# Kernel optimization log

Measured on AMD Instinct MI355X. Metric: run time of the kernel, lower is better.

Reference implementation:

```python
import jax, jax.numpy as jnp
import numpy as np

D_MODEL = 1024
NUM_HEADS = 16
DEPTH = D_MODEL // NUM_HEADS
B, S = 2, 2048


def setup_inputs() -> dict:
    key = jax.random.key(0)
    ks = jax.random.split(key, 11)
    s = 1.0 / np.sqrt(D_MODEL)
    return {
        "v": jax.random.normal(ks[0], (B, S, D_MODEL), jnp.float32),
        "k": jax.random.normal(ks[1], (B, S, D_MODEL), jnp.float32),
        "q": jax.random.normal(ks[2], (B, S, D_MODEL), jnp.float32),
        "wq": jax.random.normal(ks[3], (D_MODEL, D_MODEL), jnp.float32) * s,
        "bq": jnp.zeros((D_MODEL,), jnp.float32),
        "wk": jax.random.normal(ks[4], (D_MODEL, D_MODEL), jnp.float32) * s,
        "bk": jnp.zeros((D_MODEL,), jnp.float32),
        "wv": jax.random.normal(ks[5], (D_MODEL, D_MODEL), jnp.float32) * s,
        "bv": jnp.zeros((D_MODEL,), jnp.float32),
        "wo": jax.random.normal(ks[6], (D_MODEL, D_MODEL), jnp.float32) * s,
        "bo": jnp.zeros((D_MODEL,), jnp.float32),
    }


def _split_heads(x):
    # [B, S, D] -> [B, H, S, depth]
    b, s, _ = x.shape
    return x.reshape(b, s, NUM_HEADS, DEPTH).transpose(0, 2, 1, 3)


def reference(v, k, q, wq, bq, wk, bk, wv, bv, wo, bo):
    qh = _split_heads(q @ wq + bq)
    kh = _split_heads(k @ wk + bk)
    vh = _split_heads(v @ wv + bv)
    scale = 1.0 / jnp.sqrt(jnp.asarray(DEPTH, jnp.float32))
    logits = jnp.einsum("bhqd,bhkd->bhqk", qh, kh) * scale
    attn = jax.nn.softmax(logits, axis=-1)
    out = jnp.einsum("bhqk,bhkd->bhqd", attn, vh)
    out = out.transpose(0, 2, 1, 3).reshape(q.shape[0], -1, D_MODEL)
    return out @ wo + bo
```

## Files before the change

kernel.cpp:

```cpp
#include <hip/hip_runtime.h>
#include <hip/hip_bf16.h>
#include <math.h>

#define DM   1024
#define SEQ  2048
#define NBAT 2
#define NH   16

typedef __attribute__((ext_vector_type(8)))  short short8;
typedef __attribute__((ext_vector_type(4)))  float f32x4;
typedef __attribute__((ext_vector_type(16))) float f32x16;
typedef unsigned short ushort_t;

#define QSCALE 0.1803368801111204f
#define DEFER_THR 11.541560327111708f

__device__ __forceinline__ unsigned short f2bf(float f) {
  unsigned int u = __float_as_uint(f);
  u += 0x7fff + ((u >> 16) & 1);
  return (unsigned short)(u >> 16);
}

__device__ __forceinline__ unsigned cvtpk(float lo, float hi) {
  unsigned r;
  asm("v_cvt_pk_bf16_f32 %0, %1, %2" : "=v"(r) : "v"(lo), "v"(hi));
  return r;
}

__device__ __forceinline__ short8 mk8(unsigned a, unsigned b, unsigned c, unsigned d) {
  union { unsigned u[4]; short8 s; } x;
  x.u[0] = a; x.u[1] = b; x.u[2] = c; x.u[3] = d;
  return x.s;
}

#define GLDS16(g, l)                                                            \
  __builtin_amdgcn_global_load_lds((const __attribute__((address_space(1))) void*)(g), \
                                   (__attribute__((address_space(3))) void*)(l), 16, 0, 0)

__global__ __launch_bounds__(256) void prep(
    const float* __restrict__ q, const float* __restrict__ k, const float* __restrict__ v,
    ushort_t* __restrict__ qb, ushort_t* __restrict__ kb, ushort_t* __restrict__ vb,
    const float* __restrict__ w0, const float* __restrict__ w1,
    const float* __restrict__ w2, const float* __restrict__ w3,
    ushort_t* __restrict__ o0, ushort_t* __restrict__ o1,
    ushort_t* __restrict__ o2, ushort_t* __restrict__ o3) {
  const int z = blockIdx.y;
  const int t = threadIdx.x;
  if (z < 3) {
    const float* s = z == 0 ? q : z == 1 ? k : v;
    ushort_t* d = z == 0 ? qb : z == 1 ? kb : vb;
    int i = (blockIdx.x * 256 + t) * 8;
    f32x4 a = *(const f32x4*)(s + i);
    f32x4 b = *(const f32x4*)(s + i + 4);
    short8 o;
    o[0] = (short)f2bf(a[0]); o[1] = (short)f2bf(a[1]);
    o[2] = (short)f2bf(a[2]); o[3] = (short)f2bf(a[3]);
    o[4] = (short)f2bf(b[0]); o[5] = (short)f2bf(b[1]);
    o[6] = (short)f2bf(b[2]); o[7] = (short)f2bf(b[3]);
    *(short8*)(d + i) = o;
  } else {
    if (blockIdx.x >= 1024) return;
    const float* W = z == 3 ? w0 : z == 4 ? w1 : z == 5 ? w2 : w3;
    ushort_t* Wt = z == 3 ? o0 : z == 4 ? o1 : z == 5 ? o2 : o3;
    __shared__ float tile[32][33];
    int bx = (blockIdx.x & 31) * 32;
    int by = (blockIdx.x >> 5) * 32;
    int tx = t & 31, ty = t >> 5;
#pragma unroll
    for (int i = 0; i < 4; ++i)
      tile[ty + i * 8][tx] = W[(size_t)(by + ty + i * 8) * DM + bx + tx];
    __syncthreads();
#pragma unroll
    for (int i = 0; i < 4; ++i)
      Wt[(size_t)(bx + ty + i * 8) * DM + by + tx] = f2bf(tile[tx][ty + i * 8]);
  }
}

__global__ __launch_bounds__(256) void gemm_qkv(
    const ushort_t* __restrict__ Xq, const ushort_t* __restrict__ Xk, const ushort_t* __restrict__ Xv,
    const ushort_t* __restrict__ Wq, const ushort_t* __restrict__ Wk, const ushort_t* __restrict__ Wv,
    const float* __restrict__ Bq, const float* __restrict__ Bk, const float* __restrict__ Bv,
    ushort_t* __restrict__ Oq, ushort_t* __restrict__ Ok, ushort_t* __restrict__ Ov) {
  const int z = blockIdx.z;
  const ushort_t* X  = z == 0 ? Xq : z == 1 ? Xk : Xv;
  const ushort_t* Wt = z == 0 ? Wq : z == 1 ? Wk : Wv;
  const float* bias  = z == 0 ? Bq : z == 1 ? Bk : Bv;

  __shared__ ushort_t As[128 * 64];
  __shared__ ushort_t Bs[128 * 64];
  const int t = threadIdx.x, l = t & 63, w = t >> 6;
  const int wr = w >> 1, wc = w & 1;
  const int fr = l & 15, fg = l >> 4;
  const int mb = blockIdx.x * 128, nb = blockIdx.y * 128;

  f32x4 acc[4][4] = {};
  const int srow = w * 8 + (l >> 3);
  const int gcol = (((l & 7) ^ ((l >> 3) & 7))) * 8;

  for (int kt = 0; kt < DM; kt += 64) {
#pragma unroll
    for (int i = 0; i < 4; ++i) {
      int row = i * 32 + srow;
      GLDS16(X  + (size_t)(mb + row) * DM + kt + gcol, &As[i * 2048 + w * 512]);
      GLDS16(Wt + (size_t)(nb + row) * DM + kt + gcol, &Bs[i * 2048 + w * 512]);
    }
    __syncthreads();
#pragma unroll
    for (int ks = 0; ks < 2; ++ks) {
      short8 af[4], bf[4];
#pragma unroll
      for (int mt = 0; mt < 4; ++mt) {
        int row = wr * 64 + mt * 16 + fr;
        af[mt] = *(const short8*)&As[row * 64 + (((ks << 2) | fg) ^ (fr & 7)) * 8];
      }
#pragma unroll
      for (int nt = 0; nt < 4; ++nt) {
        int row = wc * 64 + nt * 16 + fr;
        bf[nt] = *(const short8*)&Bs[row * 64 + (((ks << 2) | fg) ^ (fr & 7)) * 8];
      }
#pragma unroll
      for (int mt = 0; mt < 4; ++mt)
#pragma unroll
        for (int nt = 0; nt < 4; ++nt)
          acc[mt][nt] = __builtin_amdgcn_mfma_f32_16x16x32_bf16(af[mt], bf[nt], acc[mt][nt], 0, 0, 0);
    }
    __syncthreads();
  }

#pragma unroll
  for (int nt = 0; nt < 4; ++nt) {
    int n = nb + wc * 64 + nt * 16 + fr;
    float bn = bias[n];
#pragma unroll
    for (int mt = 0; mt < 4; ++mt) {
#pragma unroll
      for (int r = 0; r < 4; ++r) {
        int m = mb + wr * 64 + mt * 16 + fg * 4 + r;
        float v = acc[mt][nt][r] + bn;
        if (z == 0) {
          Oq[(size_t)m * DM + n] = f2bf(v * QSCALE);
        } else if (z == 1) {
          Ok[(size_t)m * DM + n] = f2bf(v);
        } else {
          int b = m >> 11, s = m & 2047;
          int h = n >> 6, d = n & 63;
          Ov[(((size_t)(b * NH + h) * 64 + d) * SEQ) + s] = f2bf(v);
        }
      }
    }
  }
}

__global__ __launch_bounds__(256) void gemm_o(const ushort_t* __restrict__ X,
                                              const ushort_t* __restrict__ Wt,
                                              const float* __restrict__ bias,
                                              float* __restrict__ out) {
  __shared__ ushort_t As[128 * 64];
  __shared__ ushort_t Bs[64 * 64];
  const int t = threadIdx.x, l = t & 63, w = t >> 6;
  const int fr = l & 15, fg = l >> 4;
  const int mb = blockIdx.x * 128, nb = blockIdx.y * 64;

  f32x4 acc[2][4] = {};
  const int srow = w * 8 + (l >> 3);
  const int gcol = (((l & 7) ^ ((l >> 3) & 7))) * 8;

  for (int kt = 0; kt < DM; kt += 64) {
#pragma unroll
    for (int i = 0; i < 4; ++i)
      GLDS16(X + (size_t)(mb + i * 32 + srow) * DM + kt + gcol, &As[i * 2048 + w * 512]);
#pragma unroll
    for (int i = 0; i < 2; ++i)
      GLDS16(Wt + (size_t)(nb + i * 32 + srow) * DM + kt + gcol, &Bs[i * 2048 + w * 512]);
    __syncthreads();
#pragma unroll
    for (int ks = 0; ks < 2; ++ks) {
      short8 af[2], bf[4];
#pragma unroll
      for (int mt = 0; mt < 2; ++mt) {
        int row = w * 32 + mt * 16 + fr;
        af[mt] = *(const short8*)&As[row * 64 + (((ks << 2) | fg) ^ (fr & 7)) * 8];
      }
#pragma unroll
      for (int nt = 0; nt < 4; ++nt) {
        int row = nt * 16 + fr;
        bf[nt] = *(const short8*)&Bs[row * 64 + (((ks << 2) | fg) ^ (fr & 7)) * 8];
      }
#pragma unroll
      for (int mt = 0; mt < 2; ++mt)
#pragma unroll
        for (int nt = 0; nt < 4; ++nt)
          acc[mt][nt] = __builtin_amdgcn_mfma_f32_16x16x32_bf16(af[mt], bf[nt], acc[mt][nt], 0, 0, 0);
    }
    __syncthreads();
  }

#pragma unroll
  for (int nt = 0; nt < 4; ++nt) {
    int n = nb + nt * 16 + fr;
    float bn = bias[n];
#pragma unroll
    for (int mt = 0; mt < 2; ++mt)
#pragma unroll
      for (int r = 0; r < 4; ++r) {
        int m = mb + w * 32 + mt * 16 + fg * 4 + r;
        out[(size_t)m * DM + n] = acc[mt][nt][r] + bn;
      }
  }
}

#define KPAD 72
#define KVELEM (64 * KPAD)
__global__ __launch_bounds__(256) void attn_fwd(const ushort_t* __restrict__ Qh,
                                                const ushort_t* __restrict__ Kh,
                                                const ushort_t* __restrict__ Vt,
                                                ushort_t* __restrict__ Oh) {
  __shared__ ushort_t Ks[2 * KVELEM];
  __shared__ ushort_t Vs[2 * KVELEM];

  const int t = threadIdx.x, l = t & 63, w = t >> 6;
  const int col = l & 31, hi = l >> 5;
  const int q0 = blockIdx.x * 128;
  const int bh = blockIdx.y;
  const int b = bh >> 4, h = bh & 15;

  const ushort_t* Qp = Qh + (size_t)b * SEQ * DM + h * 64;
  const ushort_t* Kp = Kh + (size_t)b * SEQ * DM + h * 64;
  const ushort_t* Vp = Vt + (size_t)bh * 64 * SEQ;

  const int qrow = q0 + w * 32 + col;
  short8 qf[4];
#pragma unroll
  for (int ds = 0; ds < 4; ++ds)
    qf[ds] = *(const short8*)(Qp + (size_t)qrow * DM + ds * 16 + hi * 8);

  float m_run = -INFINITY, l_run = 0.f;
  f32x16 oA = {}, oB = {};

  const int srow = t >> 3;
  const int scol = (t & 7) * 8;

  short8 k0r = *(const short8*)(Kp + (size_t)srow * DM + scol);
  short8 k1r = *(const short8*)(Kp + (size_t)(32 + srow) * DM + scol);
  short8 v0r = *(const short8*)(Vp + (size_t)srow * SEQ + scol);
  short8 v1r = *(const short8*)(Vp + (size_t)(32 + srow) * SEQ + scol);
  *(short8*)&Ks[srow * KPAD + scol] = k0r;
  *(short8*)&Ks[(32 + srow) * KPAD + scol] = k1r;
  *(short8*)&Vs[srow * KPAD + scol] = v0r;
  *(short8*)&Vs[(32 + srow) * KPAD + scol] = v1r;
  k0r = *(const short8*)(Kp + (size_t)(64 + srow) * DM + scol);
  k1r = *(const short8*)(Kp + (size_t)(96 + srow) * DM + scol);
  v0r = *(const short8*)(Vp + (size_t)srow * SEQ + 64 + scol);
  v1r = *(const short8*)(Vp + (size_t)(32 + srow) * SEQ + 64 + scol);
  __syncthreads();

  const int NT = SEQ / 64;
  for (int kt = 0; kt < NT; ++kt) {
    const ushort_t* Kc = &Ks[(kt & 1) * KVELEM];
    const ushort_t* Vc = &Vs[(kt & 1) * KVELEM];

    f32x16 s0 = {}, s1 = {};
    __builtin_amdgcn_s_setprio(1);
#pragma unroll
    for (int ds = 0; ds < 4; ++ds) {
      short8 kf0 = *(const short8*)&Kc[col * KPAD + ds * 16 + hi * 8];
      short8 kf1 = *(const short8*)&Kc[(32 + col) * KPAD + ds * 16 + hi * 8];
      s0 = __builtin_amdgcn_mfma_f32_32x32x16_bf16(kf0, qf[ds], s0, 0, 0, 0);
      s1 = __builtin_amdgcn_mfma_f32_32x32x16_bf16(kf1, qf[ds], s1, 0, 0, 0);
    }
    __builtin_amdgcn_s_setprio(0);

    float mx = s0[0];
#pragma unroll
    for (int r = 1; r < 16; ++r) mx = fmaxf(mx, s0[r]);
#pragma unroll
    for (int r = 0; r < 16; ++r) mx = fmaxf(mx, s1[r]);
    mx = fmaxf(mx, __shfl_xor(mx, 32, 64));

    if (!__all(mx <= m_run + DEFER_THR)) {
      float nm = fmaxf(m_run, mx);
      float alpha = __builtin_amdgcn_exp2f(m_run - nm);
      m_run = nm;
      l_run *= alpha;
#pragma unroll
      for (int r = 0; r < 16; ++r) {
        float a = __shfl(alpha, (r & 3) + 8 * (r >> 2) + 4 * hi, 64);
        oA[r] *= a; oB[r] *= a;
      }
    }

    float rs = 0.f;
    float p0[16], p1[16];
#pragma unroll
    for (int r = 0; r < 16; ++r) { p0[r] = __builtin_amdgcn_exp2f(s0[r] - m_run); rs += p0[r]; }
#pragma unroll
    for (int r = 0; r < 16; ++r) { p1[r] = __builtin_amdgcn_exp2f(s1[r] - m_run); rs += p1[r]; }
    rs += __shfl_xor(rs, 32, 64);
    l_run += rs;

    unsigned wd[16];
#pragma unroll
    for (int i = 0; i < 8; ++i) wd[i] = cvtpk(p0[2 * i], p0[2 * i + 1]);
#pragma unroll
    for (int i = 0; i < 8; ++i) wd[8 + i] = cvtpk(p1[2 * i], p1[2 * i + 1]);
    unsigned rcv[8];
#pragma unroll
    for (int ksub = 0; ksub < 2; ++ksub) {
      int B = ksub * 8, R = ksub * 4;
      rcv[R + 0] = (unsigned)__shfl_xor((int)(hi ? wd[B + 0] : wd[B + 2]), 32, 64);
      rcv[R + 1] = (unsigned)__shfl_xor((int)(hi ? wd[B + 1] : wd[B + 3]), 32, 64);
      rcv[R + 2] = (unsigned)__shfl_xor((int)(hi ? wd[B + 4] : wd[B + 6]), 32, 64);
      rcv[R + 3] = (unsigned)__shfl_xor((int)(hi ? wd[B + 5] : wd[B + 7]), 32, 64);
    }
    short8 pf[4];
#pragma unroll
    for (int ks = 0; ks < 4; ++ks) {
      int B = (ks >> 1) * 8 + (ks & 1) * 4;
      int R = (ks >> 1) * 4 + (ks & 1) * 2;
      unsigned f0 = hi ? rcv[R]     : wd[B];
      unsigned f1 = hi ? rcv[R + 1] : wd[B + 1];
      unsigned f2 = hi ? wd[B + 2]  : rcv[R];
      unsigned f3 = hi ? wd[B + 3]  : rcv[R + 1];
      pf[ks] = mk8(f0, f1, f2, f3);
    }

    __builtin_amdgcn_s_setprio(1);
#pragma unroll
    for (int ks = 0; ks < 4; ++ks) {
      short8 vfA = *(const short8*)&Vc[col * KPAD + ks * 16 + hi * 8];
      short8 vfB = *(const short8*)&Vc[(32 + col) * KPAD + ks * 16 + hi * 8];
      oA = __builtin_amdgcn_mfma_f32_32x32x16_bf16(pf[ks], vfA, oA, 0, 0, 0);
      oB = __builtin_amdgcn_mfma_f32_32x32x16_bf16(pf[ks], vfB, oB, 0, 0, 0);
    }
    __builtin_amdgcn_s_setprio(0);

    if (kt + 1 < NT) {
      ushort_t* Kn = &Ks[((kt + 1) & 1) * KVELEM];
      ushort_t* Vn = &Vs[((kt + 1) & 1) * KVELEM];
      *(short8*)&Kn[srow * KPAD + scol] = k0r;
      *(short8*)&Kn[(32 + srow) * KPAD + scol] = k1r;
      *(short8*)&Vn[srow * KPAD + scol] = v0r;
      *(short8*)&Vn[(32 + srow) * KPAD + scol] = v1r;
      int kv2 = (kt + 2 < NT) ? (kt + 2) * 64 : 0;
      k0r = *(const short8*)(Kp + (size_t)(kv2 + srow) * DM + scol);
      k1r = *(const short8*)(Kp + (size_t)(kv2 + 32 + srow) * DM + scol);
      v0r = *(const short8*)(Vp + (size_t)srow * SEQ + kv2 + scol);
      v1r = *(const short8*)(Vp + (size_t)(32 + srow) * SEQ + kv2 + scol);
      __syncthreads();
    }
  }

#pragma unroll
  for (int r = 0; r < 16; ++r) {
    int qr = (r & 3) + 8 * (r >> 2) + 4 * hi;
    float li = __shfl(l_run, qr, 64);
    float inv = __builtin_amdgcn_rcpf(li);
    size_t row = (size_t)(b * SEQ + q0 + w * 32 + qr);
    Oh[row * DM + h * 64 + col]      = f2bf(oA[r] * inv);
    Oh[row * DM + h * 64 + 32 + col] = f2bf(oB[r] * inv);
  }
}

extern "C" void kernel_launch(void* const* d_in, const int* in_sizes, int n_in,
                              void* d_out, int out_size, void* d_ws, size_t ws_size,
                              hipStream_t stream) {
  const float* v  = (const float*)d_in[0];
  const float* k  = (const float*)d_in[1];
  const float* q  = (const float*)d_in[2];
  const float* wq = (const float*)d_in[3];
  const float* bq = (const float*)d_in[4];
  const float* wk = (const float*)d_in[5];
  const float* bk = (const float*)d_in[6];
  const float* wv = (const float*)d_in[7];
  const float* bv = (const float*)d_in[8];
  const float* wo = (const float*)d_in[9];
  const float* bo = (const float*)d_in[10];

  char* ws = (char*)d_ws;
  const size_t MB = 1u << 20;
  ushort_t* qb  = (ushort_t*)(ws + 0 * MB);
  ushort_t* kb  = (ushort_t*)(ws + 8 * MB);
  ushort_t* vb  = (ushort_t*)(ws + 16 * MB);
  ushort_t* wqt = (ushort_t*)(ws + 24 * MB);
  ushort_t* wkt = (ushort_t*)(ws + 26 * MB);
  ushort_t* wvt = (ushort_t*)(ws + 28 * MB);
  ushort_t* wot = (ushort_t*)(ws + 30 * MB);
  ushort_t* Qh  = (ushort_t*)(ws + 32 * MB);
  ushort_t* Kh  = (ushort_t*)(ws + 40 * MB);
  ushort_t* Vt  = (ushort_t*)(ws + 48 * MB);
  ushort_t* AO  = (ushort_t*)(ws + 56 * MB);

  prep<<<dim3(2048, 7), 256, 0, stream>>>(q, k, v, qb, kb, vb,
                                          wq, wk, wv, wo, wqt, wkt, wvt, wot);
  gemm_qkv<<<dim3(32, 8, 3), 256, 0, stream>>>(qb, kb, vb, wqt, wkt, wvt, bq, bk, bv, Qh, Kh, Vt);
  attn_fwd<<<dim3(16, 32), 256, 0, stream>>>(Qh, Kh, Vt, AO);
  gemm_o<<<dim3(32, 16), 256, 0, stream>>>(AO, wot, bo, (float*)d_out);
}
```

Measured before the change: 231.2 us.

## Double-buffer GEMM tiles and switch attention K/V staging to direct-to-LDS loads

Both projection GEMMs now use two LDS buffers and issue the next tile's direct global-to-LDS loads before computing on the current tile, so load latency overlaps the MFMA work. Attention drops the register-staged, padded K/V copies in favour of XOR-swizzled direct-to-LDS loads into double buffers. It also restructures the row-max into a tree of three-input maxes and splits the exp-sum into four accumulators to shorten dependency chains. The GEMMs now use twice the LDS per block, which may reduce occupancy. Correctness depends on the async LDS writes being complete before the single barrier at the end of each iteration.

After: 239.1 us. 1.03x slower.

```diff
diff --git a/kernel.cpp b/kernel.cpp
--- a/kernel.cpp
+++ b/kernel.cpp
@@ -14,6 +14,8 @@
 
 #define QSCALE 0.1803368801111204f
 #define DEFER_THR 11.541560327111708f
+
+#define FM3(a, b, c) fmaxf(fmaxf((a), (b)), (c))
 
 __device__ __forceinline__ unsigned short f2bf(float f) {
   unsigned int u = __float_as_uint(f);
@@ -86,8 +88,8 @@
   const ushort_t* Wt = z == 0 ? Wq : z == 1 ? Wk : Wv;
   const float* bias  = z == 0 ? Bq : z == 1 ? Bk : Bv;
 
-  __shared__ ushort_t As[128 * 64];
-  __shared__ ushort_t Bs[128 * 64];
+  __shared__ ushort_t As[2][128 * 64];
+  __shared__ ushort_t Bs[2][128 * 64];
   const int t = threadIdx.x, l = t & 63, w = t >> 6;
   const int wr = w >> 1, wc = w & 1;
   const int fr = l & 15, fg = l >> 4;
@@ -97,32 +99,40 @@
   const int srow = w * 8 + (l >> 3);
   const int gcol = (((l & 7) ^ ((l >> 3) & 7))) * 8;
 
-  for (int kt = 0; kt < DM; kt += 64) {
-#pragma unroll
-    for (int i = 0; i < 4; ++i) {
-      int row = i * 32 + srow;
-      GLDS16(X  + (size_t)(mb + row) * DM + kt + gcol, &As[i * 2048 + w * 512]);
-      GLDS16(Wt + (size_t)(nb + row) * DM + kt + gcol, &Bs[i * 2048 + w * 512]);
-    }
-    __syncthreads();
+#define QKV_STAGE(bufi, kt)                                                        \
+  _Pragma("unroll")                                                                \
+  for (int i = 0; i < 4; ++i) {                                                    \
+    int row = i * 32 + srow;                                                       \
+    GLDS16(X  + (size_t)(mb + row) * DM + (kt) + gcol, &As[bufi][i * 2048 + w * 512]); \
+    GLDS16(Wt + (size_t)(nb + row) * DM + (kt) + gcol, &Bs[bufi][i * 2048 + w * 512]); \
+  }
+
+  QKV_STAGE(0, 0);
+  __syncthreads();
+
+  for (int it = 0; it < 16; ++it) {
+    const int cur = it & 1;
+    if (it + 1 < 16) { QKV_STAGE(cur ^ 1, (it + 1) * 64); }
 #pragma unroll
     for (int ks = 0; ks < 2; ++ks) {
       short8 af[4], bf[4];
 #pragma unroll
       for (int mt = 0; mt < 4; ++mt) {
         int row = wr * 64 + mt * 16 + fr;
-        af[mt] = *(const short8*)&As[row * 64 + (((ks << 2) | fg) ^ (fr & 7)) * 8];
+        af[mt] = *(const short8*)&As[cur][row * 64 + (((ks << 2) | fg) ^ (fr & 7)) * 8];
       }
 #pragma unroll
       for (int nt = 0; nt < 4; ++nt) {
         int row = wc * 64 + nt * 16 + fr;
-        bf[nt] = *(const short8*)&Bs[row * 64 + (((ks << 2) | fg) ^ (fr & 7)) * 8];
-      }
+        bf[nt] = *(const short8*)&Bs[cur][row * 64 + (((ks << 2) | fg) ^ (fr & 7)) * 8];
+      }
+      __builtin_amdgcn_s_setprio(1);
 #pragma unroll
       for (int mt = 0; mt < 4; ++mt)
 #pragma unroll
         for (int nt = 0; nt < 4; ++nt)
           acc[mt][nt] = __builtin_amdgcn_mfma_f32_16x16x32_bf16(af[mt], bf[nt], acc[mt][nt], 0, 0, 0);
+      __builtin_amdgcn_s_setprio(0);
     }
     __syncthreads();
   }
@@ -155,8 +165,8 @@
                                               const ushort_t* __restrict__ Wt,
                                               const float* __restrict__ bias,
                                               float* __restrict__ out) {
-  __shared__ ushort_t As[128 * 64];
-  __shared__ ushort_t Bs[64 * 64];
+  __shared__ ushort_t As[2][128 * 64];
+  __shared__ ushort_t Bs[2][64 * 64];
   const int t = threadIdx.x, l = t & 63, w = t >> 6;
   const int fr = l & 15, fg = l >> 4;
   const int mb = blockIdx.x * 128, nb = blockIdx.y * 64;
@@ -165,32 +175,40 @@
   const int srow = w * 8 + (l >> 3);
   const int gcol = (((l & 7) ^ ((l >> 3) & 7))) * 8;
 
-  for (int kt = 0; kt < DM; kt += 64) {
-#pragma unroll
-    for (int i = 0; i < 4; ++i)
-      GLDS16(X + (size_t)(mb + i * 32 + srow) * DM + kt + gcol, &As[i * 2048 + w * 512]);
-#pragma unroll
-    for (int i = 0; i < 2; ++i)
-      GLDS16(Wt + (size_t)(nb + i * 32 + srow) * DM + kt + gcol, &Bs[i * 2048 + w * 512]);
-    __syncthreads();
+#define O_STAGE(bufi, kt)                                                          \
+  _Pragma("unroll")                                                                \
+  for (int i = 0; i < 4; ++i)                                                      \
+    GLDS16(X + (size_t)(mb + i * 32 + srow) * DM + (kt) + gcol, &As[bufi][i * 2048 + w * 512]); \
+  _Pragma("unroll")                                                                \
+  for (int i = 0; i < 2; ++i)                                                      \
+    GLDS16(Wt + (size_t)(nb + i * 32 + srow) * DM + (kt) + gcol, &Bs[bufi][i * 2048 + w * 512]);
+
+  O_STAGE(0, 0);
+  __syncthreads();
+
+  for (int it = 0; it < 16; ++it) {
+    const int cur = it & 1;
+    if (it + 1 < 16) { O_STAGE(cur ^ 1, (it + 1) * 64); }
 #pragma unroll
     for (int ks = 0; ks < 2; ++ks) {
       short8 af[2], bf[4];
 #pragma unroll
       for (int mt = 0; mt < 2; ++mt) {
         int row = w * 32 + mt * 16 + fr;
-        af[mt] = *(const short8*)&As[row * 64 + (((ks << 2) | fg) ^ (fr & 7)) * 8];
+        af[mt] = *(const short8*)&As[cur][row * 64 + (((ks << 2) | fg) ^ (fr & 7)) * 8];
       }
 #pragma unroll
       for (int nt = 0; nt < 4; ++nt) {
         int row = nt * 16 + fr;
-        bf[nt] = *(const short8*)&Bs[row * 64 + (((ks << 2) | fg) ^ (fr & 7)) * 8];
-      }
+        bf[nt] = *(const short8*)&Bs[cur][row * 64 + (((ks << 2) | fg) ^ (fr & 7)) * 8];
+      }
+      __builtin_amdgcn_s_setprio(1);
 #pragma unroll
       for (int mt = 0; mt < 2; ++mt)
 #pragma unroll
         for (int nt = 0; nt < 4; ++nt)
           acc[mt][nt] = __builtin_amdgcn_mfma_f32_16x16x32_bf16(af[mt], bf[nt], acc[mt][nt], 0, 0, 0);
+      __builtin_amdgcn_s_setprio(0);
     }
     __syncthreads();
   }
@@ -209,14 +227,12 @@
   }
 }
 
-#define KPAD 72
-#define KVELEM (64 * KPAD)
 __global__ __launch_bounds__(256) void attn_fwd(const ushort_t* __restrict__ Qh,
                                                 const ushort_t* __restrict__ Kh,
                                                 const ushort_t* __restrict__ Vt,
                                                 ushort_t* __restrict__ Oh) {
-  __shared__ ushort_t Ks[2 * KVELEM];
-  __shared__ ushort_t Vs[2 * KVELEM];
+  __shared__ ushort_t Ks[2][64 * 64];
+  __shared__ ushort_t Vs[2][64 * 64];
 
   const int t = threadIdx.x, l = t & 63, w = t >> 6;
   const int col = l & 31, hi = l >> 5;
@@ -237,44 +253,46 @@
   float m_run = -INFINITY, l_run = 0.f;
   f32x16 oA = {}, oB = {};
 
-  const int srow = t >> 3;
-  const int scol = (t & 7) * 8;
-
-  short8 k0r = *(const short8*)(Kp + (size_t)srow * DM + scol);
-  short8 k1r = *(const short8*)(Kp + (size_t)(32 + srow) * DM + scol);
-  short8 v0r = *(const short8*)(Vp + (size_t)srow * SEQ + scol);
-  short8 v1r = *(const short8*)(Vp + (size_t)(32 + srow) * SEQ + scol);
-  *(short8*)&Ks[srow * KPAD + scol] = k0r;
-  *(short8*)&Ks[(32 + srow) * KPAD + scol] = k1r;
-  *(short8*)&Vs[srow * KPAD + scol] = v0r;
-  *(short8*)&Vs[(32 + srow) * KPAD + scol] = v1r;
-  k0r = *(const short8*)(Kp + (size_t)(64 + srow) * DM + scol);
-  k1r = *(const short8*)(Kp + (size_t)(96 + srow) * DM + scol);
-  v0r = *(const short8*)(Vp + (size_t)srow * SEQ + 64 + scol);
-  v1r = *(const short8*)(Vp + (size_t)(32 + srow) * SEQ + 64 + scol);
+  const int srow = w * 8 + (l >> 3);
+  const int gcol = (((l & 7) ^ ((l >> 3) & 7))) * 8;
+
+#define ATTN_STAGE(bufi, kv)                                                       \
+  _Pragma("unroll")                                                                \
+  for (int i = 0; i < 2; ++i) {                                                    \
+    int row = i * 32 + srow;                                                       \
+    GLDS16(Kp + (size_t)((kv) + row) * DM + gcol, &Ks[bufi][i * 2048 + w * 512]);  \
+    GLDS16(Vp + (size_t)row * SEQ + (kv) + gcol, &Vs[bufi][i * 2048 + w * 512]);   \
+  }
+
+  ATTN_STAGE(0, 0);
   __syncthreads();
 
   const int NT = SEQ / 64;
   for (int kt = 0; kt < NT; ++kt) {
-    const ushort_t* Kc = &Ks[(kt & 1) * KVELEM];
-    const ushort_t* Vc = &Vs[(kt & 1) * KVELEM];
+    const int cur = kt & 1;
+    if (kt + 1 < NT) { ATTN_STAGE(cur ^ 1, (kt + 1) * 64); }
 
     f32x16 s0 = {}, s1 = {};
     __builtin_amdgcn_s_setprio(1);
 #pragma unroll
     for (int ds = 0; ds < 4; ++ds) {
-      short8 kf0 = *(const short8*)&Kc[col * KPAD + ds * 16 + hi * 8];
-      short8 kf1 = *(const short8*)&Kc[(32 + col) * KPAD + ds * 16 + hi * 8];
+      int c0 = ((ds * 2 + hi) ^ (col & 7)) * 8;
+      short8 kf0 = *(const short8*)&Ks[cur][col * 64 + c0];
+      short8 kf1 = *(const short8*)&Ks[cur][(32 + col) * 64 + c0];
       s0 = __builtin_amdgcn_mfma_f32_32x32x16_bf16(kf0, qf[ds], s0, 0, 0, 0);
       s1 = __builtin_amdgcn_mfma_f32_32x32x16_bf16(kf1, qf[ds], s1, 0, 0, 0);
     }
     __builtin_amdgcn_s_setprio(0);
 
-    float mx = s0[0];
-#pragma unroll
-    for (int r = 1; r < 16; ++r) mx = fmaxf(mx, s0[r]);
-#pragma unroll
-    for (int r = 0; r < 16; ++r) mx = fmaxf(mx, s1[r]);
+    float a0 = FM3(s0[0], s0[1], s0[2]),   a1 = FM3(s0[3], s0[4], s0[5]);
+    float a2 = FM3(s0[6], s0[7], s0[8]),   a3 = FM3(s0[9], s0[10], s0[11]);
+    float a4 = FM3(s0[12], s0[13], s0[14]), a5 = FM3(s0[15], s1[0], s1[1]);
+    float a6 = FM3(s1[2], s1[3], s1[4]),   a7 = FM3(s1[5], s1[6], s1[7]);
+    float a8 = FM3(s1[8], s1[9], s1[10]),  a9 = FM3(s1[11], s1[12], s1[13]);
+    float a10 = fmaxf(s1[14], s1[15]);
+    float b0 = FM3(a0, a1, a2), b1 = FM3(a3, a4, a5), b2 = FM3(a6, a7, a8);
+    float b3 = FM3(a9, a10, b0);
+    float mx = FM3(b1, b2, b3);
     mx = fmaxf(mx, __shfl_xor(mx, 32, 64));
 
     if (!__all(mx <= m_run + DEFER_THR)) {
@@ -289,12 +307,23 @@
       }
     }
 
-    float rs = 0.f;
     float p0[16], p1[16];
-#pragma unroll
-    for (int r = 0; r < 16; ++r) { p0[r] = __builtin_amdgcn_exp2f(s0[r] - m_run); rs += p0[r]; }
-#pragma unroll
-    for (int r = 0; r < 16; ++r) { p1[r] = __builtin_amdgcn_exp2f(s1[r] - m_run); rs += p1[r]; }
+    float rs0 = 0.f, rs1 = 0.f, rs2 = 0.f, rs3 = 0.f;
+#pragma unroll
+    for (int r = 0; r < 16; r += 4) {
+      p0[r] = __builtin_amdgcn_exp2f(s0[r] - m_run);     rs0 += p0[r];
+      p0[r+1] = __builtin_amdgcn_exp2f(s0[r+1] - m_run); rs1 += p0[r+1];
+      p0[r+2] = __builtin_amdgcn_exp2f(s0[r+2] - m_run); rs2 += p0[r+2];
+      p0[r+3] = __builtin_amdgcn_exp2f(s0[r+3] - m_run); rs3 += p0[r+3];
+    }
+#pragma unroll
+    for (int r = 0; r < 16; r += 4) {
+      p1[r] = __builtin_amdgcn_exp2f(s1[r] - m_run);     rs0 += p1[r];
+      p1[r+1] = __builtin_amdgcn_exp2f(s1[r+1] - m_run); rs1 += p1[r+1];
+      p1[r+2] = __builtin_amdgcn_exp2f(s1[r+2] - m_run); rs2 += p1[r+2];
+      p1[r+3] = __builtin_amdgcn_exp2f(s1[r+3] - m_run); rs3 += p1[r+3];
+    }
+    float rs = (rs0 + rs1) + (rs2 + rs3);
     rs += __shfl_xor(rs, 32, 64);
     l_run += rs;
 
@@ -327,27 +356,15 @@
     __builtin_amdgcn_s_setprio(1);
 #pragma unroll
     for (int ks = 0; ks < 4; ++ks) {
-      short8 vfA = *(const short8*)&Vc[col * KPAD + ks * 16 + hi * 8];
-      short8 vfB = *(const short8*)&Vc[(32 + col) * KPAD + ks * 16 + hi * 8];
+      int c0 = ((ks * 2 + hi) ^ (col & 7)) * 8;
+      short8 vfA = *(const short8*)&Vs[cur][col * 64 + c0];
+      short8 vfB = *(const short8*)&Vs[cur][(32 + col) * 64 + c0];
       oA = __builtin_amdgcn_mfma_f32_32x32x16_bf16(pf[ks], vfA, oA, 0, 0, 0);
       oB = __builtin_amdgcn_mfma_f32_32x32x16_bf16(pf[ks], vfB, oB, 0, 0, 0);
     }
     __builtin_amdgcn_s_setprio(0);
 
-    if (kt + 1 < NT) {
-      ushort_t* Kn = &Ks[((kt + 1) & 1) * KVELEM];
-      ushort_t* Vn = &Vs[((kt + 1) & 1) * KVELEM];
-      *(short8*)&Kn[srow * KPAD + scol] = k0r;
-      *(short8*)&Kn[(32 + srow) * KPAD + scol] = k1r;
-      *(short8*)&Vn[srow * KPAD + scol] = v0r;
-      *(short8*)&Vn[(32 + srow) * KPAD + scol] = v1r;
-      int kv2 = (kt + 2 < NT) ? (kt + 2) * 64 : 0;
-      k0r = *(const short8*)(Kp + (size_t)(kv2 + srow) * DM + scol);
-      k1r = *(const short8*)(Kp + (size_t)(kv2 + 32 + srow) * DM + scol);
-      v0r = *(const short8*)(Vp + (size_t)srow * SEQ + kv2 + scol);
-      v1r = *(const short8*)(Vp + (size_t)(32 + srow) * SEQ + kv2 + scol);
-      __syncthreads();
-    }
+    __syncthreads();
   }
 
 #pragma unroll
```

## Triple-buffer projection GEMM K-loop and shorten softmax max/sum dependency chains

Applied to the files above, without the earlier changes.

Both projection GEMMs (QKV and output) now use a three-stage LDS ring with a 32-wide K step. Loads are issued two stages ahead, and partial vmcnt waits plus a single barrier per iteration replace the load-then-sync pattern with two barriers. The attention kernel's row max is rebuilt as a tree of three-input fmax ops, and the exp sum is split across four accumulators to shorten the serial dependency chains. The costs are higher LDS use, a new swizzle pattern, and hand-placed waitcnt values that must stay correct.

Result: no change. 232.1 us (+0.4%).

```diff
diff --git a/kernel.cpp b/kernel.cpp
--- a/kernel.cpp
+++ b/kernel.cpp
@@ -15,6 +15,8 @@
 #define QSCALE 0.1803368801111204f
 #define DEFER_THR 11.541560327111708f
 
+#define FM3(a, b, c) fmaxf(fmaxf((a), (b)), (c))
+
 __device__ __forceinline__ unsigned short f2bf(float f) {
   unsigned int u = __float_as_uint(f);
   u += 0x7fff + ((u >> 16) & 1);
@@ -32,6 +34,8 @@
   x.u[0] = a; x.u[1] = b; x.u[2] = c; x.u[3] = d;
   return x.s;
 }
+
+__device__ __forceinline__ int inc3(int x) { return x == 2 ? 0 : x + 1; }
 
 #define GLDS16(g, l)                                                            \
   __builtin_amdgcn_global_load_lds((const __attribute__((address_space(1))) void*)(g), \
@@ -86,45 +90,60 @@
   const ushort_t* Wt = z == 0 ? Wq : z == 1 ? Wk : Wv;
   const float* bias  = z == 0 ? Bq : z == 1 ? Bk : Bv;
 
-  __shared__ ushort_t As[128 * 64];
-  __shared__ ushort_t Bs[128 * 64];
+  __shared__ ushort_t As[3][128 * 32];
+  __shared__ ushort_t Bs[3][128 * 32];
   const int t = threadIdx.x, l = t & 63, w = t >> 6;
   const int wr = w >> 1, wc = w & 1;
   const int fr = l & 15, fg = l >> 4;
   const int mb = blockIdx.x * 128, nb = blockIdx.y * 128;
 
   f32x4 acc[4][4] = {};
-  const int srow = w * 8 + (l >> 3);
-  const int gcol = (((l & 7) ^ ((l >> 3) & 7))) * 8;
-
-  for (int kt = 0; kt < DM; kt += 64) {
-#pragma unroll
-    for (int i = 0; i < 4; ++i) {
-      int row = i * 32 + srow;
-      GLDS16(X  + (size_t)(mb + row) * DM + kt + gcol, &As[i * 2048 + w * 512]);
-      GLDS16(Wt + (size_t)(nb + row) * DM + kt + gcol, &Bs[i * 2048 + w * 512]);
-    }
-    __syncthreads();
-#pragma unroll
-    for (int ks = 0; ks < 2; ++ks) {
-      short8 af[4], bf[4];
-#pragma unroll
-      for (int mt = 0; mt < 4; ++mt) {
-        int row = wr * 64 + mt * 16 + fr;
-        af[mt] = *(const short8*)&As[row * 64 + (((ks << 2) | fg) ^ (fr & 7)) * 8];
-      }
-#pragma unroll
-      for (int nt = 0; nt < 4; ++nt) {
-        int row = wc * 64 + nt * 16 + fr;
-        bf[nt] = *(const short8*)&Bs[row * 64 + (((ks << 2) | fg) ^ (fr & 7)) * 8];
-      }
-#pragma unroll
-      for (int mt = 0; mt < 4; ++mt)
-#pragma unroll
-        for (int nt = 0; nt < 4; ++nt)
-          acc[mt][nt] = __builtin_amdgcn_mfma_f32_16x16x32_bf16(af[mt], bf[nt], acc[mt][nt], 0, 0, 0);
-    }
-    __syncthreads();
+  const int srow = w * 16 + (l >> 2);
+  const int gcol = ((l & 3) ^ ((l >> 3) & 3)) * 8;
+
+#define QKV_STAGE(bufi, kt)                                                        \
+  _Pragma("unroll")                                                                \
+  for (int i = 0; i < 2; ++i) {                                                    \
+    int row = i * 64 + srow;                                                       \
+    GLDS16(X  + (size_t)(mb + row) * DM + (kt) + gcol, &As[bufi][i * 2048 + w * 512]); \
+    GLDS16(Wt + (size_t)(nb + row) * DM + (kt) + gcol, &Bs[bufi][i * 2048 + w * 512]); \
+  }
+
+  QKV_STAGE(0, 0);
+  QKV_STAGE(1, 32);
+  asm volatile("s_waitcnt vmcnt(4)" ::: "memory");
+  __builtin_amdgcn_s_barrier();
+  __builtin_amdgcn_sched_barrier(0);
+
+  int cur = 0, nx2 = 2;
+  const int NIT = 32;
+  for (int it = 0; it < NIT; ++it) {
+    if (it + 2 < NIT) { QKV_STAGE(nx2, (it + 2) * 32); }
+    short8 af[4], bf[4];
+#pragma unroll
+    for (int mt = 0; mt < 4; ++mt) {
+      int row = wr * 64 + mt * 16 + fr;
+      af[mt] = *(const short8*)&As[cur][row * 32 + (fg ^ ((fr >> 1) & 3)) * 8];
+    }
+#pragma unroll
+    for (int nt = 0; nt < 4; ++nt) {
+      int row = wc * 64 + nt * 16 + fr;
+      bf[nt] = *(const short8*)&Bs[cur][row * 32 + (fg ^ ((fr >> 1) & 3)) * 8];
+    }
+    __builtin_amdgcn_s_setprio(1);
+#pragma unroll
+    for (int mt = 0; mt < 4; ++mt)
+#pragma unroll
+      for (int nt = 0; nt < 4; ++nt)
+        acc[mt][nt] = __builtin_amdgcn_mfma_f32_16x16x32_bf16(af[mt], bf[nt], acc[mt][nt], 0, 0, 0);
+    __builtin_amdgcn_s_setprio(0);
+    if (it + 1 < NIT) {
+      if (it + 2 < NIT) asm volatile("s_waitcnt vmcnt(4)" ::: "memory");
+      else              asm volatile("s_waitcnt vmcnt(0)" ::: "memory");
+      __builtin_amdgcn_s_barrier();
+      __builtin_amdgcn_sched_barrier(0);
+    }
+    cur = inc3(cur); nx2 = inc3(nx2);
   }
 
 #pragma unroll
@@ -155,44 +174,57 @@
                                               const ushort_t* __restrict__ Wt,
                                               const float* __restrict__ bias,
                                               float* __restrict__ out) {
-  __shared__ ushort_t As[128 * 64];
-  __shared__ ushort_t Bs[64 * 64];
+  __shared__ ushort_t As[3][128 * 32];
+  __shared__ ushort_t Bs[3][64 * 32];
   const int t = threadIdx.x, l = t & 63, w = t >> 6;
   const int fr = l & 15, fg = l >> 4;
   const int mb = blockIdx.x * 128, nb = blockIdx.y * 64;
 
   f32x4 acc[2][4] = {};
-  const int srow = w * 8 + (l >> 3);
-  const int gcol = (((l & 7) ^ ((l >> 3) & 7))) * 8;
-
-  for (int kt = 0; kt < DM; kt += 64) {
-#pragma unroll
-    for (int i = 0; i < 4; ++i)
-      GLDS16(X + (size_t)(mb + i * 32 + srow) * DM + kt + gcol, &As[i * 2048 + w * 512]);
-#pragma unroll
-    for (int i = 0; i < 2; ++i)
-      GLDS16(Wt + (size_t)(nb + i * 32 + srow) * DM + kt + gcol, &Bs[i * 2048 + w * 512]);
-    __syncthreads();
-#pragma unroll
-    for (int ks = 0; ks < 2; ++ks) {
-      short8 af[2], bf[4];
-#pragma unroll
-      for (int mt = 0; mt < 2; ++mt) {
-        int row = w * 32 + mt * 16 + fr;
-        af[mt] = *(const short8*)&As[row * 64 + (((ks << 2) | fg) ^ (fr & 7)) * 8];
-      }
-#pragma unroll
-      for (int nt = 0; nt < 4; ++nt) {
-        int row = nt * 16 + fr;
-        bf[nt] = *(const short8*)&Bs[row * 64 + (((ks << 2) | fg) ^ (fr & 7)) * 8];
-      }
-#pragma unroll
-      for (int mt = 0; mt < 2; ++mt)
-#pragma unroll
-        for (int nt = 0; nt < 4; ++nt)
-          acc[mt][nt] = __builtin_amdgcn_mfma_f32_16x16x32_bf16(af[mt], bf[nt], acc[mt][nt], 0, 0, 0);
-    }
-    __syncthreads();
+  const int srow = w * 16 + (l >> 2);
+  const int gcol = ((l & 3) ^ ((l >> 3) & 3)) * 8;
+
+#define O_STAGE(bufi, kt)                                                          \
+  _Pragma("unroll")                                                                \
+  for (int i = 0; i < 2; ++i)                                                      \
+    GLDS16(X + (size_t)(mb + i * 64 + srow) * DM + (kt) + gcol, &As[bufi][i * 2048 + w * 512]); \
+  GLDS16(Wt + (size_t)(nb + srow) * DM + (kt) + gcol, &Bs[bufi][w * 512]);
+
+  O_STAGE(0, 0);
+  O_STAGE(1, 32);
+  asm volatile("s_waitcnt vmcnt(3)" ::: "memory");
+  __builtin_amdgcn_s_barrier();
+  __builtin_amdgcn_sched_barrier(0);
+
+  int cur = 0, nx2 = 2;
+  const int NIT = 32;
+  for (int it = 0; it < NIT; ++it) {
+    if (it + 2 < NIT) { O_STAGE(nx2, (it + 2) * 32); }
+    short8 af[2], bf[4];
+#pragma unroll
+    for (int mt = 0; mt < 2; ++mt) {
+      int row = w * 32 + mt * 16 + fr;
+      af[mt] = *(const short8*)&As[cur][row * 32 + (fg ^ ((fr >> 1) & 3)) * 8];
+    }
+#pragma unroll
+    for (int nt = 0; nt < 4; ++nt) {
+      int row = nt * 16 + fr;
+      bf[nt] = *(const short8*)&Bs[cur][row * 32 + (fg ^ ((fr >> 1) & 3)) * 8];
+    }
+    __builtin_amdgcn_s_setprio(1);
+#pragma unroll
+    for (int mt = 0; mt < 2; ++mt)
+#pragma unroll
+      for (int nt = 0; nt < 4; ++nt)
+        acc[mt][nt] = __builtin_amdgcn_mfma_f32_16x16x32_bf16(af[mt], bf[nt], acc[mt][nt], 0, 0, 0);
+    __builtin_amdgcn_s_setprio(0);
+    if (it + 1 < NIT) {
+      if (it + 2 < NIT) asm volatile("s_waitcnt vmcnt(3)" ::: "memory");
+      else              asm volatile("s_waitcnt vmcnt(0)" ::: "memory");
+      __builtin_amdgcn_s_barrier();
+      __builtin_amdgcn_sched_barrier(0);
+    }
+    cur = inc3(cur); nx2 = inc3(nx2);
   }
 
 #pragma unroll
@@ -270,11 +302,15 @@
     }
     __builtin_amdgcn_s_setprio(0);
 
-    float mx = s0[0];
-#pragma unroll
-    for (int r = 1; r < 16; ++r) mx = fmaxf(mx, s0[r]);
-#pragma unroll
-    for (int r = 0; r < 16; ++r) mx = fmaxf(mx, s1[r]);
+    float a0 = FM3(s0[0], s0[1], s0[2]),   a1 = FM3(s0[3], s0[4], s0[5]);
+    float a2 = FM3(s0[6], s0[7], s0[8]),   a3 = FM3(s0[9], s0[10], s0[11]);
+    float a4 = FM3(s0[12], s0[13], s0[14]), a5 = FM3(s0[15], s1[0], s1[1]);
+    float a6 = FM3(s1[2], s1[3], s1[4]),   a7 = FM3(s1[5], s1[6], s1[7]);
+    float a8 = FM3(s1[8], s1[9], s1[10]),  a9 = FM3(s1[11], s1[12], s1[13]);
+    float a10 = fmaxf(s1[14], s1[15]);
+    float b0 = FM3(a0, a1, a2), b1 = FM3(a3, a4, a5), b2 = FM3(a6, a7, a8);
+    float b3 = FM3(a9, a10, b0);
+    float mx = FM3(b1, b2, b3);
     mx = fmaxf(mx, __shfl_xor(mx, 32, 64));
 
     if (!__all(mx <= m_run + DEFER_THR)) {
@@ -289,12 +325,23 @@
       }
     }
 
-    float rs = 0.f;
     float p0[16], p1[16];
-#pragma unroll
-    for (int r = 0; r < 16; ++r) { p0[r] = __builtin_amdgcn_exp2f(s0[r] - m_run); rs += p0[r]; }
-#pragma unroll
-    for (int r = 0; r < 16; ++r) { p1[r] = __builtin_amdgcn_exp2f(s1[r] - m_run); rs += p1[r]; }
+    float rs0 = 0.f, rs1 = 0.f, rs2 = 0.f, rs3 = 0.f;
+#pragma unroll
+    for (int r = 0; r < 16; r += 4) {
+      p0[r] = __builtin_amdgcn_exp2f(s0[r] - m_run);     rs0 += p0[r];
+      p0[r+1] = __builtin_amdgcn_exp2f(s0[r+1] - m_run); rs1 += p0[r+1];
+      p0[r+2] = __builtin_amdgcn_exp2f(s0[r+2] - m_run); rs2 += p0[r+2];
+      p0[r+3] = __builtin_amdgcn_exp2f(s0[r+3] - m_run); rs3 += p0[r+3];
+    }
+#pragma unroll
+    for (int r = 0; r < 16; r += 4) {
+      p1[r] = __builtin_amdgcn_exp2f(s1[r] - m_run);     rs0 += p1[r];
+      p1[r+1] = __builtin_amdgcn_exp2f(s1[r+1] - m_run); rs1 += p1[r+1];
+      p1[r+2] = __builtin_amdgcn_exp2f(s1[r+2] - m_run); rs2 += p1[r+2];
+      p1[r+3] = __builtin_amdgcn_exp2f(s1[r+3] - m_run); rs3 += p1[r+3];
+    }
+    float rs = (rs0 + rs1) + (rs2 + rs3);
     rs += __shfl_xor(rs, 32, 64);
     l_run += rs;
 
```
